# Optimization experiments

Hardware: AMD Instinct MI355X
Metric: run time of the kernel (lower is better)

The kernel has to match this reference:

```python
import jax, jax.numpy as jnp
import numpy as np

EPS = 1e-08


def setup_inputs() -> dict:
    key = jax.random.key(0)
    k1, k2 = jax.random.split(key)
    # batch MUST be 1: the torch module's .view calls only succeed for batch == 1
    inp = jax.random.normal(k1, (1, 512, 256, 256), dtype=jnp.float32)
    weights = jax.random.normal(k2, (1, 512, 512, 3, 3), dtype=jnp.float32)
    return {"input": inp, "weights": weights}


def reference(input, weights):
    B, Cin, H, W = input.shape            # B == 1
    _, Cout, _, K, _ = weights.shape
    # per-output-channel demodulation: rsqrt of sum of squared weights over (in, kh, kw)
    demod = jax.lax.rsqrt(jnp.sum(weights * weights, axis=(2, 3, 4)) + EPS)  # (1, Cout)
    w = weights * demod.reshape(B, Cout, 1, 1, 1)   # (B, Cout, Cin, K, K)
    w = w.reshape(B * Cout, Cin, K, K)
    x = input.reshape(1, B * Cin, H, W)
    out = jax.lax.conv_general_dilated(
        x, w,
        window_strides=(1, 1),
        padding=[(1, 1), (1, 1)],
        rhs_dilation=(1, 1),
        dimension_numbers=("NCHW", "OIHW", "NCHW"),
        feature_group_count=B,  # grouped conv with groups = batch (here 1)
    )
    Ho, Wo = out.shape[2], out.shape[3]
    return out.reshape(B, Cout, Ho, Wo)
```

## Files before the change

### kernel.cpp

```cpp
#include <hip/hip_runtime.h>
#include <hip/hip_bf16.h>
#include <stdint.h>

#define CIN   512
#define COUT  512
#define HH    256
#define WW    256
#define NPX   (HH*WW)
#define KTAP  9

typedef __attribute__((ext_vector_type(8))) short bf16x8;
typedef __attribute__((ext_vector_type(4))) float f32x4;

__device__ __forceinline__ ushort f2bfu(float v) {
  __hip_bfloat16 b = __float2bfloat16(v);
  return *reinterpret_cast<ushort*>(&b);
}

__device__ __forceinline__ void gload_lds16(const void* g, void* l) {
  __builtin_amdgcn_global_load_lds(
      (const __attribute__((address_space(1))) uint32_t*)g,
      (__attribute__((address_space(3))) uint32_t*)l,
      16, 0, 0);
}

__global__ void demod_prep_kernel(const float* __restrict__ w,
                                  __hip_bfloat16* __restrict__ wprep) {
  const int co = blockIdx.x;
  const int t  = threadIdx.x;
  const float* wc = w + (size_t)co * (CIN * 9);

  float s = 0.f;
  for (int i = t; i < CIN * 9; i += 256) { float v = wc[i]; s += v * v; }
  #pragma unroll
  for (int off = 32; off > 0; off >>= 1) s += __shfl_down(s, off);
  __shared__ float ps[4];
  if ((t & 63) == 0) ps[t >> 6] = s;
  __syncthreads();
  const float tot = ps[0] + ps[1] + ps[2] + ps[3];
  const float d = rsqrtf(tot + 1e-8f);

  #pragma unroll
  for (int rep = 0; rep < 2; ++rep) {
    const int cin = t + rep * 256;
    float v[9];
    #pragma unroll
    for (int tap = 0; tap < 9; ++tap) v[tap] = wc[cin * 9 + tap];
    #pragma unroll
    for (int tap = 0; tap < 9; ++tap)
      wprep[(size_t)tap * (COUT * CIN) + (size_t)co * CIN + cin] =
          __float2bfloat16(v[tap] * d);
  }
}

__global__ void to_hwc_kernel(const float* __restrict__ in,
                              __hip_bfloat16* __restrict__ hwc) {
  __shared__ ushort T[64][76];
  const int bid = blockIdx.x;
  const int h  = bid >> 5;
  const int p0 = ((bid >> 3) & 3) * 64;
  const int c0 = (bid & 7) * 64;
  const int t  = threadIdx.x;

  const int pxq = (t & 15) * 4;
  const int cl  = t >> 4;
  #pragma unroll
  for (int pass = 0; pass < 4; ++pass) {
    const int c = c0 + pass * 16 + cl;
    const float4 v =
        *(const float4*)&in[(size_t)c * NPX + (size_t)h * WW + p0 + pxq];
    ushort4 u;
    u.x = f2bfu(v.x); u.y = f2bfu(v.y); u.z = f2bfu(v.z); u.w = f2bfu(v.w);
    *(ushort4*)&T[pass * 16 + cl][pxq] = u;
  }
  __syncthreads();

  const int c4 = (t & 15) * 4;
  #pragma unroll
  for (int it = 0; it < 4; ++it) {
    const int px = it * 16 + (t >> 4);
    ushort4 v;
    v.x = T[c4 + 0][px];
    v.y = T[c4 + 1][px];
    v.z = T[c4 + 2][px];
    v.w = T[c4 + 3][px];
    *(ushort4*)&hwc[((size_t)h * WW + p0 + px) * CIN + c0 + c4] = v;
  }
}

__global__ void conv_mfma_kernel(const __hip_bfloat16* __restrict__ hwc,
                                 const __hip_bfloat16* __restrict__ wprep,
                                 const __hip_bfloat16* __restrict__ zp,
                                 float* __restrict__ out) {
  __shared__ __align__(16) __hip_bfloat16 As[128 * 32];
  __shared__ __align__(16) __hip_bfloat16 Bs[128 * 32];

  const int t    = threadIdx.x;
  const int wave = t >> 6, lane = t & 63;
  const int kg   = lane >> 4, lr = lane & 15;
  const int wm   = wave >> 1, wn = wave & 1;

  const int bid = blockIdx.x;
  const int wg  = ((bid & 7) << 8) | (bid >> 3);
  const int co0 = (wg & 3) * 128;
  const int pt  = wg >> 2;
  const int h   = pt >> 1;
  const int w0  = (pt & 1) * 128;

  const int srow = t >> 2;
  const int scol = (t & 3) * 8;

  __hip_bfloat16* Ab0 = &As[(wave * 64) * 8];
  __hip_bfloat16* Ab1 = &As[(256 + wave * 64) * 8];
  __hip_bfloat16* Bb0 = &Bs[(wave * 64) * 8];
  __hip_bfloat16* Bb1 = &Bs[(256 + wave * 64) * 8];

  f32x4 acc[4][4] = {};

  for (int tap = 0; tap < KTAP; ++tap) {
    const int dh = tap / 3 - 1, dw = tap % 3 - 1;
    const int hp = h + dh;
    if (hp < 0 || hp >= HH) continue;

    const __hip_bfloat16* gw =
        wprep + (size_t)tap * (COUT * CIN) + (size_t)(co0 + srow) * CIN + scol;

    const int wc0 = w0 + dw + srow;
    const int wc1 = wc0 + 64;
    const bool v0 = ((unsigned)wc0 < (unsigned)WW);
    const bool v1 = ((unsigned)wc1 < (unsigned)WW);
    const __hip_bfloat16* gb0 = hwc + ((long)hp * WW + wc0) * CIN + scol;
    const __hip_bfloat16* gb1 = hwc + ((long)hp * WW + wc1) * CIN + scol;

    for (int k0 = 0; k0 < CIN; k0 += 32) {
      __syncthreads();
      gload_lds16(gw + k0,             Ab0);
      gload_lds16(gw + k0 + 64 * CIN,  Ab1);
      gload_lds16(v0 ? (const void*)(gb0 + k0) : (const void*)zp, Bb0);
      gload_lds16(v1 ? (const void*)(gb1 + k0) : (const void*)zp, Bb1);
      __syncthreads();

      bf16x8 af[4], bf[4];
      #pragma unroll
      for (int mi = 0; mi < 4; ++mi)
        af[mi] = *(const bf16x8*)&As[(wm * 64 + mi * 16 + lr) * 32 + kg * 8];
      #pragma unroll
      for (int ni = 0; ni < 4; ++ni)
        bf[ni] = *(const bf16x8*)&Bs[(wn * 64 + ni * 16 + lr) * 32 + kg * 8];

      #pragma unroll
      for (int mi = 0; mi < 4; ++mi)
        #pragma unroll
        for (int ni = 0; ni < 4; ++ni)
          acc[mi][ni] = __builtin_amdgcn_mfma_f32_16x16x32_bf16(
              af[mi], bf[ni], acc[mi][ni], 0, 0, 0);
    }
  }

  const long pxbase = (long)h * WW + w0;
  #pragma unroll
  for (int mi = 0; mi < 4; ++mi) {
    const int row = co0 + wm * 64 + mi * 16 + kg * 4;
    #pragma unroll
    for (int ni = 0; ni < 4; ++ni) {
      const long col = pxbase + wn * 64 + ni * 16 + lr;
      #pragma unroll
      for (int j = 0; j < 4; ++j)
        out[(long)(row + j) * NPX + col] = acc[mi][ni][j];
    }
  }
}

extern "C" void kernel_launch(void* const* d_in, const int* in_sizes, int n_in,
                              void* d_out, int out_size, void* d_ws, size_t ws_size,
                              hipStream_t stream) {
  const float* inp = (const float*)d_in[0];
  const float* wts = (const float*)d_in[1];
  float* out = (float*)d_out;

  char* ws = (char*)d_ws;
  __hip_bfloat16* hwc   = (__hip_bfloat16*)ws;
  __hip_bfloat16* wprep = (__hip_bfloat16*)(ws + (size_t)NPX * CIN * 2);
  __hip_bfloat16* zp    = (__hip_bfloat16*)(ws + (size_t)NPX * CIN * 2
                                               + (size_t)KTAP * COUT * CIN * 2);

  (void)hipMemsetAsync(zp, 0, 256, stream);

  demod_prep_kernel<<<COUT, 256, 0, stream>>>(wts, wprep);
  to_hwc_kernel<<<HH * 32, 256, 0, stream>>>(inp, hwc);
  conv_mfma_kernel<<<(COUT / 128) * (NPX / 128), 256, 0, stream>>>(hwc, wprep, zp, out);
}
```

Before: 575.4 us.

## Rewrite conv GEMM as 256x256 tile, 8-wave, double-buffered pipelined MFMA kernel

Replaces the 128x128-tile, single-buffered conv kernel with a 256x256 tile (one full output row of 256 pixels by 256 output channels) computed by 8 waves. LDS operands are double-buffered with XOR-swizzled layout, and global-to-LDS loads for the next K slice are issued between MFMA phases with explicit vmcnt waits and setprio. Boundary rows skip zero taps up front instead of per-iteration. This targets the load/compute serialization and the barrier stalls of the old loop, and raises arithmetic intensity. In exchange it uses much more LDS (128KB) and registers, and the grid drops to 512 blocks.

Result: faster. 557.9 us (-3.0%).

```diff
diff --git a/kernel.cpp b/kernel.cpp
--- a/kernel.cpp
+++ b/kernel.cpp
@@ -88,87 +88,136 @@
   }
 }
 
-__global__ void conv_mfma_kernel(const __hip_bfloat16* __restrict__ hwc,
-                                 const __hip_bfloat16* __restrict__ wprep,
-                                 const __hip_bfloat16* __restrict__ zp,
-                                 float* __restrict__ out) {
-  __shared__ __align__(16) __hip_bfloat16 As[128 * 32];
-  __shared__ __align__(16) __hip_bfloat16 Bs[128 * 32];
+__global__ __launch_bounds__(512, 2)
+void conv_mfma8_kernel(const __hip_bfloat16* __restrict__ hwc,
+                       const __hip_bfloat16* __restrict__ wprep,
+                       const __hip_bfloat16* __restrict__ zp,
+                       float* __restrict__ out) {
+  __shared__ __align__(16) ushort Al[2][2][128 * 64];
+  __shared__ __align__(16) ushort Bl[2][2][128 * 64];
 
   const int t    = threadIdx.x;
-  const int wave = t >> 6, lane = t & 63;
-  const int kg   = lane >> 4, lr = lane & 15;
-  const int wm   = wave >> 1, wn = wave & 1;
+  const int lane = t & 63, kg = lane >> 4, lr = lane & 15;
+  const int wave = t >> 6, wm = wave >> 2, wn = wave & 3;
+  const int wuni = t & ~63;
 
   const int bid = blockIdx.x;
-  const int wg  = ((bid & 7) << 8) | (bid >> 3);
-  const int co0 = (wg & 3) * 128;
-  const int pt  = wg >> 2;
-  const int h   = pt >> 1;
-  const int w0  = (pt & 1) * 128;
-
-  const int srow = t >> 2;
-  const int scol = (t & 3) * 8;
-
-  __hip_bfloat16* Ab0 = &As[(wave * 64) * 8];
-  __hip_bfloat16* Ab1 = &As[(256 + wave * 64) * 8];
-  __hip_bfloat16* Bb0 = &Bs[(wave * 64) * 8];
-  __hip_bfloat16* Bb1 = &Bs[(256 + wave * 64) * 8];
-
-  f32x4 acc[4][4] = {};
-
-  for (int tap = 0; tap < KTAP; ++tap) {
-    const int dh = tap / 3 - 1, dw = tap % 3 - 1;
-    const int hp = h + dh;
-    if (hp < 0 || hp >= HH) continue;
-
-    const __hip_bfloat16* gw =
-        wprep + (size_t)tap * (COUT * CIN) + (size_t)(co0 + srow) * CIN + scol;
-
-    const int wc0 = w0 + dw + srow;
-    const int wc1 = wc0 + 64;
-    const bool v0 = ((unsigned)wc0 < (unsigned)WW);
-    const bool v1 = ((unsigned)wc1 < (unsigned)WW);
-    const __hip_bfloat16* gb0 = hwc + ((long)hp * WW + wc0) * CIN + scol;
-    const __hip_bfloat16* gb1 = hwc + ((long)hp * WW + wc1) * CIN + scol;
-
-    for (int k0 = 0; k0 < CIN; k0 += 32) {
-      __syncthreads();
-      gload_lds16(gw + k0,             Ab0);
-      gload_lds16(gw + k0 + 64 * CIN,  Ab1);
-      gload_lds16(v0 ? (const void*)(gb0 + k0) : (const void*)zp, Bb0);
-      gload_lds16(v1 ? (const void*)(gb1 + k0) : (const void*)zp, Bb1);
-      __syncthreads();
-
-      bf16x8 af[4], bf[4];
+  const int wg  = ((bid & 7) << 6) | (bid >> 3);
+  const int co0 = (wg & 1) * 256;
+  const int h   = wg >> 1;
+
+  const int tap_base = (h == 0) ? 3 : 0;
+  const int nv  = (h == 0 || h == HH - 1) ? 6 : 9;
+  const int NTK = nv * 8;
+  const int iters = NTK >> 1;
+
+  const ushort* __restrict__ W = (const ushort*)wprep;
+  const ushort* __restrict__ X = (const ushort*)hwc;
+
+  auto stageA = [&](int kt, int mh, int buf) {
+    const int tap = tap_base + (kt >> 3);
+    const int k0  = (kt & 7) * 64;
+    const ushort* wp = W + (size_t)tap * (COUT * CIN) + k0;
+    #pragma unroll
+    for (int j = 0; j < 2; ++j) {
+      const int c   = j * 512 + t;
+      const int row = c >> 3;
+      const int co  = co0 + ((row >> 6) << 7) + mh * 64 + (row & 63);
+      const int cg8 = ((c & 7) ^ (row & 7)) << 3;
+      gload_lds16(wp + (size_t)co * CIN + cg8,
+                  &Al[buf][mh][(j * 512 + wuni) * 8]);
+    }
+  };
+  auto stageB = [&](int kt, int nh, int buf) {
+    const int tap = tap_base + (kt >> 3);
+    const int k0  = (kt & 7) * 64;
+    const int d3  = tap / 3;
+    const int dw  = tap - d3 * 3 - 1;
+    const int hp  = h + d3 - 1;
+    const ushort* bp = X + (size_t)hp * WW * CIN + k0;
+    #pragma unroll
+    for (int j = 0; j < 2; ++j) {
+      const int c   = j * 512 + t;
+      const int row = c >> 3;
+      const int px  = ((row >> 5) << 6) + nh * 32 + (row & 31);
+      const int cg8 = ((c & 7) ^ (row & 7)) << 3;
+      const int pxs = px + dw;
+      const ushort* src = ((unsigned)pxs < (unsigned)WW)
+                        ? bp + (size_t)pxs * CIN + cg8
+                        : (const ushort*)zp;
+      gload_lds16(src, &Bl[buf][nh][(j * 512 + wuni) * 8]);
+    }
+  };
+
+  f32x4 acc[8][4] = {};
+
+  stageA(0, 0, 0); stageA(0, 1, 0); stageB(0, 0, 0); stageB(0, 1, 0);
+  stageA(1, 0, 1); stageB(1, 0, 1);
+  asm volatile("s_waitcnt vmcnt(4)" ::: "memory");
+  __builtin_amdgcn_s_barrier();
+
+#define PHASE(MH, NH, BUF, STAGE_STMT, VM_STMT) do {                          \
+    bf16x8 af[4][2], bf[2][2];                                                \
+    _Pragma("unroll") for (int mi = 0; mi < 4; ++mi)                          \
+      _Pragma("unroll") for (int kk = 0; kk < 2; ++kk)                        \
+        af[mi][kk] = *(const bf16x8*)&Al[BUF][MH][                            \
+            ((wm * 64 + mi * 16 + lr) * 64 + kk * 32 + kg * 8)                \
+            ^ ((lr & 7) << 3)];                                               \
+    _Pragma("unroll") for (int nj = 0; nj < 2; ++nj)                          \
+      _Pragma("unroll") for (int kk = 0; kk < 2; ++kk)                        \
+        bf[nj][kk] = *(const bf16x8*)&Bl[BUF][NH][                            \
+            ((wn * 32 + nj * 16 + lr) * 64 + kk * 32 + kg * 8)                \
+            ^ ((lr & 7) << 3)];                                               \
+    STAGE_STMT;                                                               \
+    __builtin_amdgcn_s_barrier();                                             \
+    asm volatile("s_waitcnt lgkmcnt(0)" ::: "memory");                        \
+    __builtin_amdgcn_sched_barrier(0);                                        \
+    __builtin_amdgcn_s_setprio(1);                                            \
+    _Pragma("unroll") for (int mi = 0; mi < 4; ++mi)                          \
+      _Pragma("unroll") for (int nj = 0; nj < 2; ++nj)                        \
+        _Pragma("unroll") for (int kk = 0; kk < 2; ++kk)                      \
+          acc[MH * 4 + mi][NH * 2 + nj] =                                     \
+              __builtin_amdgcn_mfma_f32_16x16x32_bf16(                        \
+                  af[mi][kk], bf[nj][kk], acc[MH * 4 + mi][NH * 2 + nj],      \
+                  0, 0, 0);                                                   \
+    __builtin_amdgcn_s_setprio(0);                                            \
+    VM_STMT;                                                                  \
+    __builtin_amdgcn_s_barrier();                                             \
+  } while (0)
+
+  for (int it = 0; it < iters; ++it) {
+    const int ka = 2 * it + 1;
+    const int kb = (2 * it + 2 < NTK) ? 2 * it + 2 : NTK - 1;
+    const int kc = (2 * it + 3 < NTK) ? 2 * it + 3 : NTK - 1;
+    PHASE(0, 0, 0, stageA(ka, 1, 1), );
+    PHASE(0, 1, 0, stageB(ka, 1, 1), );
+    PHASE(1, 0, 0, stageA(kb, 0, 0), );
+    PHASE(1, 1, 0, stageB(kb, 0, 0),
+          asm volatile("s_waitcnt vmcnt(4)" ::: "memory"));
+    PHASE(0, 0, 1, stageA(kb, 1, 0), );
+    PHASE(0, 1, 1, stageB(kb, 1, 0), );
+    PHASE(1, 0, 1, stageA(kc, 0, 1), );
+    PHASE(1, 1, 1, stageB(kc, 0, 1),
+          asm volatile("s_waitcnt vmcnt(4)" ::: "memory"));
+  }
+#undef PHASE
+
+  const size_t pxb = (size_t)h * WW;
+  #pragma unroll
+  for (int mh = 0; mh < 2; ++mh)
+    #pragma unroll
+    for (int mi = 0; mi < 4; ++mi) {
+      const int r0 = co0 + wm * 128 + mh * 64 + mi * 16 + kg * 4;
       #pragma unroll
-      for (int mi = 0; mi < 4; ++mi)
-        af[mi] = *(const bf16x8*)&As[(wm * 64 + mi * 16 + lr) * 32 + kg * 8];
-      #pragma unroll
-      for (int ni = 0; ni < 4; ++ni)
-        bf[ni] = *(const bf16x8*)&Bs[(wn * 64 + ni * 16 + lr) * 32 + kg * 8];
-
-      #pragma unroll
-      for (int mi = 0; mi < 4; ++mi)
+      for (int nh = 0; nh < 2; ++nh)
         #pragma unroll
-        for (int ni = 0; ni < 4; ++ni)
-          acc[mi][ni] = __builtin_amdgcn_mfma_f32_16x16x32_bf16(
-              af[mi], bf[ni], acc[mi][ni], 0, 0, 0);
+        for (int nj = 0; nj < 2; ++nj) {
+          const int px = wn * 64 + nh * 32 + nj * 16 + lr;
+          #pragma unroll
+          for (int j = 0; j < 4; ++j)
+            out[(size_t)(r0 + j) * NPX + pxb + px] = acc[mh * 4 + mi][nh * 2 + nj][j];
+        }
     }
-  }
-
-  const long pxbase = (long)h * WW + w0;
-  #pragma unroll
-  for (int mi = 0; mi < 4; ++mi) {
-    const int row = co0 + wm * 64 + mi * 16 + kg * 4;
-    #pragma unroll
-    for (int ni = 0; ni < 4; ++ni) {
-      const long col = pxbase + wn * 64 + ni * 16 + lr;
-      #pragma unroll
-      for (int j = 0; j < 4; ++j)
-        out[(long)(row + j) * NPX + col] = acc[mi][ni][j];
-    }
-  }
 }
 
 extern "C" void kernel_launch(void* const* d_in, const int* in_sizes, int n_in,
@@ -188,5 +237,5 @@
 
   demod_prep_kernel<<<COUT, 256, 0, stream>>>(wts, wprep);
   to_hwc_kernel<<<HH * 32, 256, 0, stream>>>(inp, hwc);
-  conv_mfma_kernel<<<(COUT / 128) * (NPX / 128), 256, 0, stream>>>(hwc, wprep, zp, out);
-}
+  conv_mfma8_kernel<<<512, 512, 0, stream>>>(hwc, wprep, zp, out);
+}
```
